# Optimization experiments

Hardware: AMD Instinct MI355X
Metric: run time of the kernel (lower is better)

Reference implementation:

```python
import jax, jax.numpy as jnp
import numpy as np

B, T, PHYS = 256, 64, 3        # batch of initial conditions, time steps, physical dim
LAT, NN, NHID = 8, 128, 3      # latent dim, hidden width, num hidden layers
WIN, PRED = 32, 64             # Hankel window, num_pred_steps


def _mlp(x, w_in, b_in, w_h, b_h, w_out, b_out):
    # Dense stack: relu hidden layers, linear output (ae_output_activation='linear')
    h = jax.nn.relu(x @ w_in + b_in)
    for i in range(w_h.shape[0]):
        h = jax.nn.relu(h @ w_h[i] + b_h[i])
    return h @ w_out + b_out


def _hankel_dmd(y):
    # y: [B, L, T] latent trajectories (already transposed as in call())
    Bsz, L, Tn = y.shape
    R = Tn - (WIN - 1)                                   # num_rows_hankel
    # Vectorized Hankel build (replaces nested TensorArray loops):
    idx = jnp.arange(R)[:, None] + jnp.arange(WIN)[None, :]
    H = y[:, :, idx].reshape(Bsz, L * R, WIN)
    Ym, Yp = H[:, :, :-1], H[:, :, 1:]
    # Exact DMD operator A = Yp V Sig^-1 U^H (full M x M, as in the TF code)
    U, sig, Vh = jnp.linalg.svd(Ym, full_matrices=False)
    V = jnp.swapaxes(Vh, -1, -2)
    A = Yp @ (V / sig[:, None, :]) @ jnp.swapaxes(U, -1, -2)     # [B, M, M]
    A = jax.lax.stop_gradient(A)   # no-op in fwd; eig has no JAX grad rule
    evals, evecs = jnp.linalg.eig(A)                             # complex64: [B,M], [B,M,M]
    Phi = jnp.linalg.solve(evecs, Ym.astype(evecs.dtype))
    y0 = Phi[:, :, 0]                                            # [B, M]
    evecs_s = evecs[:, ::R, :]                                   # stride = R -> [B, L, M]
    # Vectorized replacement of the sequential recon loop: evals^k for k=0..P-1
    powers = evals[:, None, :] ** jnp.arange(PRED)[None, :, None]  # [B, P, M]
    modes = powers * y0[:, None, :]                                # [B, P, M]
    recon = jnp.real(jnp.einsum('blm,bpm->bpl', evecs_s, modes))   # [B, P, L]
    return recon


def setup_inputs() -> dict:
    ks = jax.random.split(jax.random.key(0), 8)

    def w(k, fi, fo):
        return jax.random.normal(k, (fi, fo), jnp.float32) / np.sqrt(fi)

    def wh(k, f):
        return jax.random.normal(k, (NHID, f, f), jnp.float32) / np.sqrt(f)

    return {
        'x': jax.random.normal(ks[0], (B, T, PHYS), jnp.float32),
        'enc_w_in': w(ks[1], PHYS, NN), 'enc_b_in': jnp.zeros((NN,), jnp.float32),
        'enc_w_h': wh(ks[2], NN), 'enc_b_h': jnp.zeros((NHID, NN), jnp.float32),
        'enc_w_out': w(ks[3], NN, LAT), 'enc_b_out': jnp.zeros((LAT,), jnp.float32),
        'dec_w_in': w(ks[4], LAT, NN), 'dec_b_in': jnp.zeros((NN,), jnp.float32),
        'dec_w_h': wh(ks[5], NN), 'dec_b_h': jnp.zeros((NHID, NN), jnp.float32),
        'dec_w_out': w(ks[6], NN, PHYS), 'dec_b_out': jnp.zeros((PHYS,), jnp.float32),
    }


def reference(x, enc_w_in, enc_b_in, enc_w_h, enc_b_h, enc_w_out, enc_b_out,
              dec_w_in, dec_b_in, dec_w_h, dec_b_h, dec_w_out, dec_b_out):
    y = _mlp(x, enc_w_in, enc_b_in, enc_w_h, enc_b_h, enc_w_out, enc_b_out)        # [B, T, LAT]
    x_ae = _mlp(y, dec_w_in, dec_b_in, dec_w_h, dec_b_h, dec_w_out, dec_b_out)     # [B, T, PHYS]
    y_adv = _hankel_dmd(jnp.swapaxes(y, 1, 2))                                     # [B, PRED, LAT]
    x_adv = _mlp(y_adv, dec_w_in, dec_b_in, dec_w_h, dec_b_h, dec_w_out, dec_b_out)  # [B, PRED, PHYS]
    return (y, x_ae, x_adv, y_adv)
```

## Files before the change

### kernel.cpp

```cpp
#include <hip/hip_runtime.h>
#include <math.h>

namespace {
constexpr int kB = 256;
constexpr int kT = 64;
constexpr int kPhys = 3;
constexpr int kLat = 8;
constexpr int kNN = 128;
constexpr int kWin = 32;
constexpr int kPred = 64;
constexpr int kHRow = 132;
constexpr int kThreads = 1024;
constexpr int kWUnit = 8 * 4 * 64 * 8;
}

typedef short bf16x8 __attribute__((ext_vector_type(8)));
typedef float f32x4 __attribute__((ext_vector_type(4)));

__device__ __forceinline__ double rdlane_f64(double x, int l) {
  const long long v = __double_as_longlong(x);
  const int lo = __builtin_amdgcn_readlane((int)(unsigned int)(v & 0xffffffffll), l);
  const int hi = __builtin_amdgcn_readlane((int)(v >> 32), l);
  const long long r = (((long long)hi) << 32) | (unsigned long long)(unsigned int)lo;
  return __longlong_as_double(r);
}

__device__ __forceinline__ unsigned rneb(float f) {
  const unsigned u = __float_as_uint(f);
  return (u + 0x7fffu + ((u >> 16) & 1u)) >> 16;
}
__device__ __forceinline__ void split3(float a, short& s1, short& s2, short& s3) {
  const unsigned b1 = rneb(a);
  const float f1 = __uint_as_float(b1 << 16);
  const float r1 = a - f1;
  const unsigned b2 = rneb(r1);
  const float f2 = __uint_as_float(b2 << 16);
  s1 = (short)b1; s2 = (short)b2; s3 = (short)rneb(r1 - f2);
}
__device__ __forceinline__ void split2(float a, short& s1, short& s2) {
  const unsigned b1 = rneb(a);
  const float f1 = __uint_as_float(b1 << 16);
  s1 = (short)b1; s2 = (short)rneb(a - f1);
}

__global__ __launch_bounds__(256) void split_weights_kernel(
    const float* __restrict__ ewh, const float* __restrict__ dwh,
    short* __restrict__ wfrag)
{
  const int gid = blockIdx.x * 256 + threadIdx.x;
  const int l = gid & 63;
  const int q = (gid >> 6) & 3;
  const int n = (gid >> 8) & 7;
  const int layer = gid >> 11;
  const bool enc = layer < 3;
  const float* __restrict__ W = enc ? (ewh + (size_t)layer * kNN * kNN)
                                    : (dwh + (size_t)(layer - 3) * kNN * kNN);
  const int colg = 16 * n + (l & 15);
  const int krow = 8 * (l >> 4);
  bf16x8 p1, p2, p3;
#pragma unroll
  for (int e = 0; e < 8; ++e) {
    const float wv = W[(32 * q + krow + e) * kNN + colg];
    short s1, s2, s3; split3(wv, s1, s2, s3);
    p1[e] = s1; p2[e] = s2; p3[e] = s3;
  }
  const int off = ((n * 4 + q) * 64 + l) * 8;
  if (enc) {
    const size_t base = (size_t)(layer * 3) * kWUnit;
    *(bf16x8*)&wfrag[base + off] = p1;
    *(bf16x8*)&wfrag[base + kWUnit + off] = p2;
    *(bf16x8*)&wfrag[base + 2 * kWUnit + off] = p3;
  } else {
    const size_t base = (size_t)(9 + (layer - 3) * 2) * kWUnit;
    *(bf16x8*)&wfrag[base + off] = p1;
    *(bf16x8*)&wfrag[base + kWUnit + off] = p2;
  }
}

template<int MPW, int SPLITS, bool TO_FRAG>
__device__ __forceinline__ void mfma_enc(
    const short* __restrict__ Bfrag, const float* __restrict__ bias,
    const short* __restrict__ fragIn, void* __restrict__ out, int tid)
{
  constexpr int MT = 2 * MPW;
  constexpr int PLANE = MT * 4 * 64 * 8;
  const int w = tid >> 6, l = tid & 63;
  const int n = w & 7, m0 = (w >> 3) * MPW;
  const int colg = 16 * n + (l & 15);
  bf16x8 B1[4], B2[4], B3[4];
#pragma unroll
  for (int q = 0; q < 4; ++q) {
    const int boff = ((n * 4 + q) * 64 + l) * 8;
    B1[q] = *(const bf16x8*)&Bfrag[boff];
    B2[q] = *(const bf16x8*)&Bfrag[kWUnit + boff];
    if constexpr (SPLITS == 3) B3[q] = *(const bf16x8*)&Bfrag[2 * kWUnit + boff];
  }
  const float bj = bias[colg];
  f32x4 acc[MPW];
#pragma unroll
  for (int mi = 0; mi < MPW; ++mi) acc[mi] = {bj, bj, bj, bj};
#pragma unroll
  for (int q = 0; q < 4; ++q) {
#pragma unroll
    for (int mi = 0; mi < MPW; ++mi) {
      const int o = (((m0 + mi) * 4 + q) * 64 + l) * 8;
      const bf16x8 a1 = *(const bf16x8*)&fragIn[o];
      const bf16x8 a2 = *(const bf16x8*)&fragIn[PLANE + o];
      acc[mi] = __builtin_amdgcn_mfma_f32_16x16x32_bf16(a1, B1[q], acc[mi], 0, 0, 0);
      acc[mi] = __builtin_amdgcn_mfma_f32_16x16x32_bf16(a1, B2[q], acc[mi], 0, 0, 0);
      acc[mi] = __builtin_amdgcn_mfma_f32_16x16x32_bf16(a2, B1[q], acc[mi], 0, 0, 0);
      if constexpr (SPLITS == 3) {
        const bf16x8 a3 = *(const bf16x8*)&fragIn[2 * PLANE + o];
        acc[mi] = __builtin_amdgcn_mfma_f32_16x16x32_bf16(a1, B3[q], acc[mi], 0, 0, 0);
        acc[mi] = __builtin_amdgcn_mfma_f32_16x16x32_bf16(a2, B2[q], acc[mi], 0, 0, 0);
        acc[mi] = __builtin_amdgcn_mfma_f32_16x16x32_bf16(a3, B1[q], acc[mi], 0, 0, 0);
      }
    }
  }
  const int rbase = (l >> 4) * 4;
  if constexpr (TO_FRAG) {
    short* __restrict__ f = (short*)out;
    const int qt = colg >> 5, sub = (colg >> 3) & 3, et = colg & 7;
#pragma unroll
    for (int mi = 0; mi < MPW; ++mi)
#pragma unroll
      for (int r = 0; r < 4; ++r) {
        const float v = fmaxf(acc[mi][r], 0.f);
        const int off = (((m0 + mi) * 4 + qt) * 64 + (rbase + r + 16 * sub)) * 8 + et;
        short s1, s2, s3; split3(v, s1, s2, s3);
        f[off] = s1; f[PLANE + off] = s2; f[2 * PLANE + off] = s3;
      }
  } else {
    float* __restrict__ hb = (float*)out;
#pragma unroll
    for (int mi = 0; mi < MPW; ++mi)
#pragma unroll
      for (int r = 0; r < 4; ++r)
        hb[(16 * (m0 + mi) + rbase + r) * kHRow + colg] = fmaxf(acc[mi][r], 0.f);
  }
}

template<int MTN, bool TO_FRAG>
__device__ __forceinline__ void mfma_dec(
    const short* __restrict__ Bfrag, const float* __restrict__ bias,
    const short* __restrict__ fragIn, void* __restrict__ out, int n, int l)
{
  constexpr int PLANE = MTN * 4 * 64 * 8;
  const int colg = 16 * n + (l & 15);
  bf16x8 B1[4], B2[4];
#pragma unroll
  for (int q = 0; q < 4; ++q) {
    const int boff = ((n * 4 + q) * 64 + l) * 8;
    B1[q] = *(const bf16x8*)&Bfrag[boff];
    B2[q] = *(const bf16x8*)&Bfrag[kWUnit + boff];
  }
  const float bj = bias[colg];
  f32x4 acc[MTN];
#pragma unroll
  for (int mi = 0; mi < MTN; ++mi) acc[mi] = {bj, bj, bj, bj};
#pragma unroll
  for (int q = 0; q < 4; ++q) {
#pragma unroll
    for (int mi = 0; mi < MTN; ++mi) {
      const int o = ((mi * 4 + q) * 64 + l) * 8;
      const bf16x8 a1 = *(const bf16x8*)&fragIn[o];
      const bf16x8 a2 = *(const bf16x8*)&fragIn[PLANE + o];
      acc[mi] = __builtin_amdgcn_mfma_f32_16x16x32_bf16(a1, B1[q], acc[mi], 0, 0, 0);
      acc[mi] = __builtin_amdgcn_mfma_f32_16x16x32_bf16(a1, B2[q], acc[mi], 0, 0, 0);
      acc[mi] = __builtin_amdgcn_mfma_f32_16x16x32_bf16(a2, B1[q], acc[mi], 0, 0, 0);
    }
  }
  const int rbase = (l >> 4) * 4;
  if constexpr (TO_FRAG) {
    short* __restrict__ f = (short*)out;
    const int qt = colg >> 5, sub = (colg >> 3) & 3, et = colg & 7;
#pragma unroll
    for (int mi = 0; mi < MTN; ++mi)
#pragma unroll
      for (int r = 0; r < 4; ++r) {
        const float v = fmaxf(acc[mi][r], 0.f);
        const int off = ((mi * 4 + qt) * 64 + (rbase + r + 16 * sub)) * 8 + et;
        short s1, s2; split2(v, s1, s2);
        f[off] = s1; f[PLANE + off] = s2;
      }
  } else {
    float* __restrict__ hb = (float*)out;
#pragma unroll
    for (int mi = 0; mi < MTN; ++mi)
#pragma unroll
      for (int r = 0; r < 4; ++r)
        hb[(16 * mi + rbase + r) * kHRow + colg] = fmaxf(acc[mi][r], 0.f);
  }
}

__global__ __launch_bounds__(kThreads, 4) void fused_kernel(
    const float* __restrict__ x,
    const float* __restrict__ ewin, const float* __restrict__ ebin,
    const float* __restrict__ ebh,
    const float* __restrict__ ewout,const float* __restrict__ ebout,
    const float* __restrict__ dwin, const float* __restrict__ dbin,
    const float* __restrict__ dbh,
    const float* __restrict__ dwout,const float* __restrict__ dbout,
    const short* __restrict__ wfrag,
    float* __restrict__ y_g, float* __restrict__ xae_g,
    float* __restrict__ xadv_g, float* __restrict__ yadv_g)
{
  __shared__ __align__(16) char bufA[50688];
  __shared__ __align__(16) char bufB[50688];
  __shared__ __align__(16) double dmdS[5280];
  __shared__ float ybuf[512];
  __shared__ float yadv2[256];
  __shared__ float xstash[192];

  double* P    = dmdS;
  double* Corr = dmdS + 2144;
  double* KTm  = dmdS + 3200;
  double* Dv   = dmdS + 4223;

  short* fragA_G1 = (short*)bufA;
  short* fragA_G2 = (short*)(bufA + 32768);
  short* fragB_G1 = (short*)bufB;
  short* fragB_G2 = (short*)(bufB + 33792);
  float* hbB_G1   = (float*)bufB;
  float* hbA_G2   = (float*)bufA;

  const int tid = threadIdx.x;
  const int l64 = tid & 63;
  const int b = blockIdx.x;

  {
    constexpr int PE = 4 * 4 * 64 * 8;
    short* __restrict__ f = (short*)bufA;
    const float* __restrict__ xg = x + (size_t)b * kT * kPhys;
    const int j = tid & 127, rg = tid >> 7;
    const float w0 = ewin[j], w1 = ewin[kNN + j], w2 = ewin[2 * kNN + j];
    const float bj = ebin[j];
    const int qt = j >> 5, sub = (j >> 3) & 3, et = j & 7;
#pragma unroll
    for (int rr = 0; rr < 8; ++rr) {
      const int r = rg * 8 + rr;
      const float* __restrict__ xr = xg + r * 3;
      const float a = fmaxf(bj + xr[0] * w0 + xr[1] * w1 + xr[2] * w2, 0.f);
      short s1, s2, s3; split3(a, s1, s2, s3);
      const int off = (((r >> 4) * 4 + qt) * 64 + ((r & 15) + 16 * sub)) * 8 + et;
      f[off] = s1; f[PE + off] = s2; f[2 * PE + off] = s3;
    }
  }
  __syncthreads();

  mfma_enc<2, 3, true >(wfrag + (size_t)0 * kWUnit, ebh + 0 * kNN, (short*)bufA, bufB, tid);
  __syncthreads();
  mfma_enc<2, 3, true >(wfrag + (size_t)3 * kWUnit, ebh + 1 * kNN, (short*)bufB, bufA, tid);
  __syncthreads();
  mfma_enc<2, 3, false>(wfrag + (size_t)6 * kWUnit, ebh + 2 * kNN, (short*)bufA, bufB, tid);
  __syncthreads();

  if (tid < 512) {
    const float* __restrict__ hb = (const float*)bufB;
    const int r = tid >> 3, o = tid & 7;
    float a = ebout[o];
    for (int k4 = 0; k4 < kNN; k4 += 4) {
      const float4 hv = *(const float4*)&hb[r * kHRow + k4];
      a += hv.x * ewout[(k4 + 0) * kLat + o] + hv.y * ewout[(k4 + 1) * kLat + o]
         + hv.z * ewout[(k4 + 2) * kLat + o] + hv.w * ewout[(k4 + 3) * kLat + o];
    }
    ybuf[tid] = a;
  }
  __syncthreads();

  if (tid < 512) {
    for (int idx = tid; idx < 32 * 64; idx += 512) {
      const int d = idx >> 6, t = idx & 63;
      if (t + d < kT) {
        double s = 0.0;
#pragma unroll
        for (int l = 0; l < kLat; ++l)
          s += (double)ybuf[t * 8 + l] * (double)ybuf[(t + d) * 8 + l];
        P[d * 67 + t] = s;
      }
    }
  } else {
    constexpr int PD = 4 * 4 * 64 * 8;
    short* __restrict__ f = fragA_G1;
    const int j = tid & 127, rg = (tid >> 7) - 4;
    float wr[kLat];
#pragma unroll
    for (int k = 0; k < kLat; ++k) wr[k] = dwin[k * kNN + j];
    const float bj = dbin[j];
    const int qt = j >> 5, sub = (j >> 3) & 3, et = j & 7;
#pragma unroll
    for (int rr = 0; rr < 16; ++rr) {
      const int r = rg * 16 + rr;
      const float* __restrict__ src = &ybuf[r * kLat];
      float a = bj;
#pragma unroll
      for (int k = 0; k < kLat; ++k) a += src[k] * wr[k];
      a = fmaxf(a, 0.f);
      short s1, s2; split2(a, s1, s2);
      const int off = (((r >> 4) * 4 + qt) * 64 + ((r & 15) + 16 * sub)) * 8 + et;
      f[off] = s1; f[PD + off] = s2;
    }
  }
  __syncthreads();

  {
    const int a = tid >> 5, c = tid & 31;
    const int d = (c >= a) ? (c - a) : (a - c);
    const int base = (c >= a) ? a : c;
    double s0 = 0.0, s1 = 0.0;
#pragma unroll
    for (int r = 0; r < 32; r += 2) { s0 += P[d * 67 + base + r]; s1 += P[d * 67 + base + r + 1]; }
    Corr[a * 33 + c] = s0 + s1 + P[d * 67 + base + 32];
  }
  __syncthreads();

  if (tid < 64) {
    const int lane = tid;
    const int colidx = (lane <= 30) ? lane : (lane <= 61 ? lane - 30 : 1);
    double m[31];
#pragma unroll
    for (int i = 0; i < 31; ++i) m[i] = Corr[i * 33 + colidx];
#pragma unroll
    for (int k = 0; k < 31; ++k) {
      const double piv = rdlane_f64(m[k], k);
      const double pinv = 1.0 / piv;
      m[k] *= pinv;
#pragma unroll
      for (int i = 0; i < 31; ++i) {
        if (i == k) continue;
        const double bci = rdlane_f64(m[i], k);
        m[i] = fma(-bci, m[k], m[i]);
      }
    }
    if (lane >= 31 && lane < 62) {
      const int c = lane - 31;
#pragma unroll
      for (int i = 0; i < 31; ++i) KTm[i * 33 + c] = m[i];
    }
    const int ri = (lane < 31) ? lane : 0;
    double Kr[31];
#pragma unroll
    for (int j = 0; j < 31; ++j) Kr[j] = KTm[ri * 33 + j];
    double dv = Kr[30];
    if (lane < 31) Dv[0 * 33 + lane] = dv;
    for (int k = 0; k < 31; ++k) {
      double a0 = 0.0, a1 = 0.0, a2 = 0.0, a3 = 0.0;
#pragma unroll
      for (int j = 0; j < 31; ++j) {
        const double dj = rdlane_f64(dv, j);
        if ((j & 3) == 0) a0 = fma(Kr[j], dj, a0);
        else if ((j & 3) == 1) a1 = fma(Kr[j], dj, a1);
        else if ((j & 3) == 2) a2 = fma(Kr[j], dj, a2);
        else a3 = fma(Kr[j], dj, a3);
      }
      dv = (a0 + a1) + (a2 + a3);
      if (lane < 31) Dv[(k + 1) * 33 + lane] = dv;
    }
  } else if (tid >= 512) {
    mfma_dec<4, true>(wfrag + (size_t)9 * kWUnit, dbh + 0 * kNN,
                      fragA_G1, fragB_G1, (tid >> 6) - 8, l64);
  }
  __syncthreads();

  if (tid < 512) {
    mfma_dec<4, true>(wfrag + (size_t)11 * kWUnit, dbh + 1 * kNN,
                      fragB_G1, fragA_G1, tid >> 6, l64);
  } else if (tid < 768) {
    const int q = tid - 512;
    const int k = q >> 3, l = q & 7;
    double a0 = 0.0, a1 = 0.0, a2 = 0.0, a3 = 0.0;
#pragma unroll
    for (int j = 0; j < 31; ++j) {
      const double t = (double)ybuf[(j + 1) * 8 + l];
      if ((j & 3) == 0) a0 = fma(t, Dv[k * 33 + j], a0);
      else if ((j & 3) == 1) a1 = fma(t, Dv[k * 33 + j], a1);
      else if ((j & 3) == 2) a2 = fma(t, Dv[k * 33 + j], a2);
      else a3 = fma(t, Dv[k * 33 + j], a3);
    }
    yadv2[q] = (float)((a0 + a1) + (a2 + a3));
  }
  __syncthreads();

  if (tid < 512) {
    mfma_dec<4, false>(wfrag + (size_t)13 * kWUnit, dbh + 2 * kNN,
                       fragA_G1, hbB_G1, tid >> 6, l64);
  } else {
    constexpr int PD = 2 * 4 * 64 * 8;
    short* __restrict__ f = fragA_G2;
    const int j = tid & 127, rg = (tid >> 7) - 4;
    float wr[kLat];
#pragma unroll
    for (int k = 0; k < kLat; ++k) wr[k] = dwin[k * kNN + j];
    const float bj = dbin[j];
    const int qt = j >> 5, sub = (j >> 3) & 3, et = j & 7;
#pragma unroll
    for (int rr = 0; rr < 8; ++rr) {
      const int r = 64 + rg * 8 + rr;
      const float* __restrict__ src = &yadv2[(r - kT) * kLat];
      float a = bj;
#pragma unroll
      for (int k = 0; k < kLat; ++k) a += src[k] * wr[k];
      a = fmaxf(a, 0.f);
      short s1, s2; split2(a, s1, s2);
      const int mi = (r - 64) >> 4;
      const int off = ((mi * 4 + qt) * 64 + ((r & 15) + 16 * sub)) * 8 + et;
      f[off] = s1; f[PD + off] = s2;
    }
  }
  __syncthreads();

  if (tid < 192) {
    const int r = tid / 3, o = tid - r * 3;
    float a = dbout[o];
    for (int k4 = 0; k4 < kNN; k4 += 4) {
      const float4 hv = *(const float4*)&hbB_G1[r * kHRow + k4];
      a += hv.x * dwout[(k4 + 0) * kPhys + o] + hv.y * dwout[(k4 + 1) * kPhys + o]
         + hv.z * dwout[(k4 + 2) * kPhys + o] + hv.w * dwout[(k4 + 3) * kPhys + o];
    }
    xstash[tid] = a;
  } else if (tid >= 512) {
    mfma_dec<2, true>(wfrag + (size_t)9 * kWUnit, dbh + 0 * kNN,
                      fragA_G2, fragB_G2, (tid >> 6) - 8, l64);
  }
  __syncthreads();

  if (tid >= 512) {
    mfma_dec<2, true>(wfrag + (size_t)11 * kWUnit, dbh + 1 * kNN,
                      fragB_G2, fragA_G2, (tid >> 6) - 8, l64);
  }
  __syncthreads();

  if (tid < 512) {
    mfma_dec<2, false>(wfrag + (size_t)13 * kWUnit, dbh + 2 * kNN,
                       fragA_G2, hbA_G2, tid >> 6, l64);
  }
  __syncthreads();

  if (tid < 96) {
    const int r = tid / 3, o = tid - r * 3;
    float a = dbout[o];
    for (int k4 = 0; k4 < kNN; k4 += 4) {
      const float4 hv = *(const float4*)&hbA_G2[r * kHRow + k4];
      a += hv.x * dwout[(k4 + 0) * kPhys + o] + hv.y * dwout[(k4 + 1) * kPhys + o]
         + hv.z * dwout[(k4 + 2) * kPhys + o] + hv.w * dwout[(k4 + 3) * kPhys + o];
    }
    xadv_g[(size_t)b * kT * kPhys + (r + 32) * kPhys + o] = a;
  } else {
    for (int i = tid - 96; i < 192 + 512 + 512; i += kThreads - 96) {
      if (i < 192) {
        xae_g[(size_t)b * kT * kPhys + i] = xstash[i];
        if (i < 96) xadv_g[(size_t)b * kT * kPhys + i] = xstash[i];
      } else if (i < 704) {
        const int q = i - 192;
        yadv_g[(size_t)b * kPred * kLat + q] = (q < 256) ? ybuf[q] : yadv2[q - 256];
      } else {
        const int q = i - 704;
        y_g[(size_t)b * kT * kLat + q] = ybuf[q];
      }
    }
  }
}

extern "C" void kernel_launch(void* const* d_in, const int* in_sizes, int n_in,
                              void* d_out, int out_size, void* d_ws, size_t ws_size,
                              hipStream_t stream)
{
  const float* x         = (const float*)d_in[0];
  const float* enc_w_in  = (const float*)d_in[1];
  const float* enc_b_in  = (const float*)d_in[2];
  const float* enc_w_h   = (const float*)d_in[3];
  const float* enc_b_h   = (const float*)d_in[4];
  const float* enc_w_out = (const float*)d_in[5];
  const float* enc_b_out = (const float*)d_in[6];
  const float* dec_w_in  = (const float*)d_in[7];
  const float* dec_b_in  = (const float*)d_in[8];
  const float* dec_w_h   = (const float*)d_in[9];
  const float* dec_b_h   = (const float*)d_in[10];
  const float* dec_w_out = (const float*)d_in[11];
  const float* dec_b_out = (const float*)d_in[12];

  float* out   = (float*)d_out;
  float* y     = out;
  float* x_ae  = out + (size_t)kB * kT * kLat;
  float* x_adv = x_ae + (size_t)kB * kT * kPhys;
  float* y_adv = x_adv + (size_t)kB * kT * kPhys;

  short* wfrag = (short*)d_ws;

  split_weights_kernel<<<48, 256, 0, stream>>>(enc_w_h, dec_w_h, wfrag);
  fused_kernel<<<kB, kThreads, 0, stream>>>(
      x, enc_w_in, enc_b_in, enc_b_h, enc_w_out, enc_b_out,
      dec_w_in, dec_b_in, dec_b_h, dec_w_out, dec_b_out,
      wfrag, y, x_ae, x_adv, y_adv);
}
```

Measured before the change: 55.38 us.

## Prefetch MFMA weight fragments into registers ahead of each layer and remap decoder waves

Weight B-fragments for each encoder and decoder layer are now loaded into registers one stage early, so the global loads overlap the previous layer's MFMAs instead of sitting at the start of each layer. All decoder MLP layers are moved onto the upper 512 threads, and the yadv, input-layer and output-store work is reassigned to the lower threads so the two halves run concurrently. The final global stores are split across stages. This raises register pressure, since several B4 register sets are live at once, which could lower occupancy or cause spills.

```diff
diff --git a/kernel.cpp b/kernel.cpp
--- a/kernel.cpp
+++ b/kernel.cpp
@@ -41,6 +41,14 @@
   const unsigned b1 = rneb(a);
   const float f1 = __uint_as_float(b1 << 16);
   s1 = (short)b1; s2 = (short)rneb(a - f1);
+}
+
+struct B4 { bf16x8 v[4]; };
+__device__ __forceinline__ void loadPlane(B4& d, const short* __restrict__ plane,
+                                          int n, int l) {
+#pragma unroll
+  for (int q = 0; q < 4; ++q)
+    d.v[q] = *(const bf16x8*)&plane[((n * 4 + q) * 64 + l) * 8];
 }
 
 __global__ __launch_bounds__(256) void split_weights_kernel(
@@ -77,44 +85,33 @@
   }
 }
 
-template<int MPW, int SPLITS, bool TO_FRAG>
-__device__ __forceinline__ void mfma_enc(
-    const short* __restrict__ Bfrag, const float* __restrict__ bias,
+template<bool TO_FRAG>
+__device__ __forceinline__ void mfma_enc3(
+    const B4& b1, const B4& b2, const B4& b3, const float* __restrict__ bias,
     const short* __restrict__ fragIn, void* __restrict__ out, int tid)
 {
-  constexpr int MT = 2 * MPW;
-  constexpr int PLANE = MT * 4 * 64 * 8;
+  constexpr int PLANE = 4 * 4 * 64 * 8;
   const int w = tid >> 6, l = tid & 63;
-  const int n = w & 7, m0 = (w >> 3) * MPW;
+  const int n = w & 7, m0 = (w >> 3) * 2;
   const int colg = 16 * n + (l & 15);
-  bf16x8 B1[4], B2[4], B3[4];
+  const float bj = bias[colg];
+  f32x4 acc[2];
+#pragma unroll
+  for (int mi = 0; mi < 2; ++mi) acc[mi] = {bj, bj, bj, bj};
 #pragma unroll
   for (int q = 0; q < 4; ++q) {
-    const int boff = ((n * 4 + q) * 64 + l) * 8;
-    B1[q] = *(const bf16x8*)&Bfrag[boff];
-    B2[q] = *(const bf16x8*)&Bfrag[kWUnit + boff];
-    if constexpr (SPLITS == 3) B3[q] = *(const bf16x8*)&Bfrag[2 * kWUnit + boff];
-  }
-  const float bj = bias[colg];
-  f32x4 acc[MPW];
-#pragma unroll
-  for (int mi = 0; mi < MPW; ++mi) acc[mi] = {bj, bj, bj, bj};
-#pragma unroll
-  for (int q = 0; q < 4; ++q) {
-#pragma unroll
-    for (int mi = 0; mi < MPW; ++mi) {
+#pragma unroll
+    for (int mi = 0; mi < 2; ++mi) {
       const int o = (((m0 + mi) * 4 + q) * 64 + l) * 8;
       const bf16x8 a1 = *(const bf16x8*)&fragIn[o];
       const bf16x8 a2 = *(const bf16x8*)&fragIn[PLANE + o];
-      acc[mi] = __builtin_amdgcn_mfma_f32_16x16x32_bf16(a1, B1[q], acc[mi], 0, 0, 0);
-      acc[mi] = __builtin_amdgcn_mfma_f32_16x16x32_bf16(a1, B2[q], acc[mi], 0, 0, 0);
-      acc[mi] = __builtin_amdgcn_mfma_f32_16x16x32_bf16(a2, B1[q], acc[mi], 0, 0, 0);
-      if constexpr (SPLITS == 3) {
-        const bf16x8 a3 = *(const bf16x8*)&fragIn[2 * PLANE + o];
-        acc[mi] = __builtin_amdgcn_mfma_f32_16x16x32_bf16(a1, B3[q], acc[mi], 0, 0, 0);
-        acc[mi] = __builtin_amdgcn_mfma_f32_16x16x32_bf16(a2, B2[q], acc[mi], 0, 0, 0);
-        acc[mi] = __builtin_amdgcn_mfma_f32_16x16x32_bf16(a3, B1[q], acc[mi], 0, 0, 0);
-      }
+      const bf16x8 a3 = *(const bf16x8*)&fragIn[2 * PLANE + o];
+      acc[mi] = __builtin_amdgcn_mfma_f32_16x16x32_bf16(a1, b1.v[q], acc[mi], 0, 0, 0);
+      acc[mi] = __builtin_amdgcn_mfma_f32_16x16x32_bf16(a1, b2.v[q], acc[mi], 0, 0, 0);
+      acc[mi] = __builtin_amdgcn_mfma_f32_16x16x32_bf16(a2, b1.v[q], acc[mi], 0, 0, 0);
+      acc[mi] = __builtin_amdgcn_mfma_f32_16x16x32_bf16(a1, b3.v[q], acc[mi], 0, 0, 0);
+      acc[mi] = __builtin_amdgcn_mfma_f32_16x16x32_bf16(a2, b2.v[q], acc[mi], 0, 0, 0);
+      acc[mi] = __builtin_amdgcn_mfma_f32_16x16x32_bf16(a3, b1.v[q], acc[mi], 0, 0, 0);
     }
   }
   const int rbase = (l >> 4) * 4;
@@ -122,7 +119,7 @@
     short* __restrict__ f = (short*)out;
     const int qt = colg >> 5, sub = (colg >> 3) & 3, et = colg & 7;
 #pragma unroll
-    for (int mi = 0; mi < MPW; ++mi)
+    for (int mi = 0; mi < 2; ++mi)
 #pragma unroll
       for (int r = 0; r < 4; ++r) {
         const float v = fmaxf(acc[mi][r], 0.f);
@@ -133,7 +130,7 @@
   } else {
     float* __restrict__ hb = (float*)out;
 #pragma unroll
-    for (int mi = 0; mi < MPW; ++mi)
+    for (int mi = 0; mi < 2; ++mi)
 #pragma unroll
       for (int r = 0; r < 4; ++r)
         hb[(16 * (m0 + mi) + rbase + r) * kHRow + colg] = fmaxf(acc[mi][r], 0.f);
@@ -141,19 +138,12 @@
 }
 
 template<int MTN, bool TO_FRAG>
-__device__ __forceinline__ void mfma_dec(
-    const short* __restrict__ Bfrag, const float* __restrict__ bias,
+__device__ __forceinline__ void mfma_dec2(
+    const B4& b1, const B4& b2, const float* __restrict__ bias,
     const short* __restrict__ fragIn, void* __restrict__ out, int n, int l)
 {
   constexpr int PLANE = MTN * 4 * 64 * 8;
   const int colg = 16 * n + (l & 15);
-  bf16x8 B1[4], B2[4];
-#pragma unroll
-  for (int q = 0; q < 4; ++q) {
-    const int boff = ((n * 4 + q) * 64 + l) * 8;
-    B1[q] = *(const bf16x8*)&Bfrag[boff];
-    B2[q] = *(const bf16x8*)&Bfrag[kWUnit + boff];
-  }
   const float bj = bias[colg];
   f32x4 acc[MTN];
 #pragma unroll
@@ -165,9 +155,9 @@
       const int o = ((mi * 4 + q) * 64 + l) * 8;
       const bf16x8 a1 = *(const bf16x8*)&fragIn[o];
       const bf16x8 a2 = *(const bf16x8*)&fragIn[PLANE + o];
-      acc[mi] = __builtin_amdgcn_mfma_f32_16x16x32_bf16(a1, B1[q], acc[mi], 0, 0, 0);
-      acc[mi] = __builtin_amdgcn_mfma_f32_16x16x32_bf16(a1, B2[q], acc[mi], 0, 0, 0);
-      acc[mi] = __builtin_amdgcn_mfma_f32_16x16x32_bf16(a2, B1[q], acc[mi], 0, 0, 0);
+      acc[mi] = __builtin_amdgcn_mfma_f32_16x16x32_bf16(a1, b1.v[q], acc[mi], 0, 0, 0);
+      acc[mi] = __builtin_amdgcn_mfma_f32_16x16x32_bf16(a1, b2.v[q], acc[mi], 0, 0, 0);
+      acc[mi] = __builtin_amdgcn_mfma_f32_16x16x32_bf16(a2, b1.v[q], acc[mi], 0, 0, 0);
     }
   }
   const int rbase = (l >> 4) * 4;
@@ -224,9 +214,21 @@
   float* hbB_G1   = (float*)bufB;
   float* hbA_G2   = (float*)bufA;
 
+  const short* wE0 = wfrag;
+  const short* wE1 = wfrag + (size_t)3 * kWUnit;
+  const short* wE2 = wfrag + (size_t)6 * kWUnit;
+  const short* wD0 = wfrag + (size_t)9 * kWUnit;
+  const short* wD1 = wfrag + (size_t)11 * kWUnit;
+  const short* wD2 = wfrag + (size_t)13 * kWUnit;
+
   const int tid = threadIdx.x;
   const int l64 = tid & 63;
+  const int nE = (tid >> 6) & 7;
+  const int nD = (tid >> 6) - 8;
   const int b = blockIdx.x;
+
+  B4 S0p1, S0p2, S1p1, S1p2, T;
+  B4 C0p1, C0p2, C1p1, C1p2;
 
   {
     constexpr int PE = 4 * 4 * 64 * 8;
@@ -236,6 +238,9 @@
     const float w0 = ewin[j], w1 = ewin[kNN + j], w2 = ewin[2 * kNN + j];
     const float bj = ebin[j];
     const int qt = j >> 5, sub = (j >> 3) & 3, et = j & 7;
+    loadPlane(S0p1, wE0, nE, l64);
+    loadPlane(S0p2, wE0 + kWUnit, nE, l64);
+    loadPlane(T, wE0 + 2 * kWUnit, nE, l64);
 #pragma unroll
     for (int rr = 0; rr < 8; ++rr) {
       const int r = rg * 8 + rr;
@@ -248,11 +253,19 @@
   }
   __syncthreads();
 
-  mfma_enc<2, 3, true >(wfrag + (size_t)0 * kWUnit, ebh + 0 * kNN, (short*)bufA, bufB, tid);
-  __syncthreads();
-  mfma_enc<2, 3, true >(wfrag + (size_t)3 * kWUnit, ebh + 1 * kNN, (short*)bufB, bufA, tid);
-  __syncthreads();
-  mfma_enc<2, 3, false>(wfrag + (size_t)6 * kWUnit, ebh + 2 * kNN, (short*)bufA, bufB, tid);
+  loadPlane(S1p1, wE1, nE, l64);
+  loadPlane(S1p2, wE1 + kWUnit, nE, l64);
+  mfma_enc3<true>(S0p1, S0p2, T, ebh + 0 * kNN, (short*)bufA, bufB, tid);
+  loadPlane(T, wE1 + 2 * kWUnit, nE, l64);
+  __syncthreads();
+
+  loadPlane(S0p1, wE2, nE, l64);
+  loadPlane(S0p2, wE2 + kWUnit, nE, l64);
+  mfma_enc3<true>(S1p1, S1p2, T, ebh + 1 * kNN, (short*)bufB, bufA, tid);
+  loadPlane(T, wE2 + 2 * kWUnit, nE, l64);
+  __syncthreads();
+
+  mfma_enc3<false>(S0p1, S0p2, T, ebh + 2 * kNN, (short*)bufA, bufB, tid);
   __syncthreads();
 
   if (tid < 512) {
@@ -265,6 +278,9 @@
          + hv.z * ewout[(k4 + 2) * kLat + o] + hv.w * ewout[(k4 + 3) * kLat + o];
     }
     ybuf[tid] = a;
+  } else {
+    loadPlane(C0p1, wD0, nD, l64);
+    loadPlane(C0p2, wD0 + kWUnit, nD, l64);
   }
   __syncthreads();
 
@@ -357,17 +373,14 @@
       if (lane < 31) Dv[(k + 1) * 33 + lane] = dv;
     }
   } else if (tid >= 512) {
-    mfma_dec<4, true>(wfrag + (size_t)9 * kWUnit, dbh + 0 * kNN,
-                      fragA_G1, fragB_G1, (tid >> 6) - 8, l64);
-  }
-  __syncthreads();
-
-  if (tid < 512) {
-    mfma_dec<4, true>(wfrag + (size_t)11 * kWUnit, dbh + 1 * kNN,
-                      fragB_G1, fragA_G1, tid >> 6, l64);
-  } else if (tid < 768) {
-    const int q = tid - 512;
-    const int k = q >> 3, l = q & 7;
+    loadPlane(C1p1, wD1, nD, l64);
+    loadPlane(C1p2, wD1 + kWUnit, nD, l64);
+    mfma_dec2<4, true>(C0p1, C0p2, dbh + 0 * kNN, fragA_G1, fragB_G1, nD, l64);
+  }
+  __syncthreads();
+
+  if (tid < 256) {
+    const int k = tid >> 3, l = tid & 7;
     double a0 = 0.0, a1 = 0.0, a2 = 0.0, a3 = 0.0;
 #pragma unroll
     for (int j = 0; j < 31; ++j) {
@@ -377,17 +390,18 @@
       else if ((j & 3) == 2) a2 = fma(t, Dv[k * 33 + j], a2);
       else a3 = fma(t, Dv[k * 33 + j], a3);
     }
-    yadv2[q] = (float)((a0 + a1) + (a2 + a3));
+    yadv2[tid] = (float)((a0 + a1) + (a2 + a3));
+  } else if (tid >= 512) {
+    loadPlane(C0p1, wD2, nD, l64);
+    loadPlane(C0p2, wD2 + kWUnit, nD, l64);
+    mfma_dec2<4, true>(C1p1, C1p2, dbh + 1 * kNN, fragB_G1, fragA_G1, nD, l64);
   }
   __syncthreads();
 
   if (tid < 512) {
-    mfma_dec<4, false>(wfrag + (size_t)13 * kWUnit, dbh + 2 * kNN,
-                       fragA_G1, hbB_G1, tid >> 6, l64);
-  } else {
     constexpr int PD = 2 * 4 * 64 * 8;
     short* __restrict__ f = fragA_G2;
-    const int j = tid & 127, rg = (tid >> 7) - 4;
+    const int j = tid & 127, rg = tid >> 7;
     float wr[kLat];
 #pragma unroll
     for (int k = 0; k < kLat; ++k) wr[k] = dwin[k * kNN + j];
@@ -406,6 +420,10 @@
       const int off = ((mi * 4 + qt) * 64 + ((r & 15) + 16 * sub)) * 8 + et;
       f[off] = s1; f[PD + off] = s2;
     }
+  } else {
+    loadPlane(C1p1, wD0, nD, l64);
+    loadPlane(C1p2, wD0 + kWUnit, nD, l64);
+    mfma_dec2<4, false>(C0p1, C0p2, dbh + 2 * kNN, fragA_G1, hbB_G1, nD, l64);
   }
   __syncthreads();
 
@@ -419,20 +437,24 @@
     }
     xstash[tid] = a;
   } else if (tid >= 512) {
-    mfma_dec<2, true>(wfrag + (size_t)9 * kWUnit, dbh + 0 * kNN,
-                      fragA_G2, fragB_G2, (tid >> 6) - 8, l64);
+    loadPlane(C0p1, wD1, nD, l64);
+    loadPlane(C0p2, wD1 + kWUnit, nD, l64);
+    mfma_dec2<2, true>(C1p1, C1p2, dbh + 0 * kNN, fragA_G2, fragB_G2, nD, l64);
+  }
+  __syncthreads();
+
+  if (tid < 512) {
+    y_g[(size_t)b * kT * kLat + tid] = ybuf[tid];
+    yadv_g[(size_t)b * kPred * kLat + tid] = (tid < 256) ? ybuf[tid] : yadv2[tid - 256];
+  } else {
+    loadPlane(C1p1, wD2, nD, l64);
+    loadPlane(C1p2, wD2 + kWUnit, nD, l64);
+    mfma_dec2<2, true>(C0p1, C0p2, dbh + 1 * kNN, fragB_G2, fragA_G2, nD, l64);
   }
   __syncthreads();
 
   if (tid >= 512) {
-    mfma_dec<2, true>(wfrag + (size_t)11 * kWUnit, dbh + 1 * kNN,
-                      fragB_G2, fragA_G2, (tid >> 6) - 8, l64);
-  }
-  __syncthreads();
-
-  if (tid < 512) {
-    mfma_dec<2, false>(wfrag + (size_t)13 * kWUnit, dbh + 2 * kNN,
-                       fragA_G2, hbA_G2, tid >> 6, l64);
+    mfma_dec2<2, false>(C1p1, C1p2, dbh + 2 * kNN, fragA_G2, hbA_G2, nD, l64);
   }
   __syncthreads();
 
@@ -445,19 +467,12 @@
          + hv.z * dwout[(k4 + 2) * kPhys + o] + hv.w * dwout[(k4 + 3) * kPhys + o];
     }
     xadv_g[(size_t)b * kT * kPhys + (r + 32) * kPhys + o] = a;
-  } else {
-    for (int i = tid - 96; i < 192 + 512 + 512; i += kThreads - 96) {
-      if (i < 192) {
-        xae_g[(size_t)b * kT * kPhys + i] = xstash[i];
-        if (i < 96) xadv_g[(size_t)b * kT * kPhys + i] = xstash[i];
-      } else if (i < 704) {
-        const int q = i - 192;
-        yadv_g[(size_t)b * kPred * kLat + q] = (q < 256) ? ybuf[q] : yadv2[q - 256];
-      } else {
-        const int q = i - 704;
-        y_g[(size_t)b * kT * kLat + q] = ybuf[q];
-      }
-    }
+  } else if (tid < 288) {
+    const int i = tid - 96;
+    xae_g[(size_t)b * kT * kPhys + i] = xstash[i];
+  } else if (tid < 384) {
+    const int i = tid - 288;
+    xadv_g[(size_t)b * kT * kPhys + i] = xstash[i];
   }
 }
 
```

Measured after the change: 58.64 us. +5.9%, slower.
